# Performance work log

Hardware: AMD Instinct MI355X
Metric: run time of the kernel (lower is better)

## Reference

```python
import jax, jax.numpy as jnp
import numpy as np

EPS = 1e-6
BANDWIDTH = 10


def _norm_last(x):
    return x / jnp.sum(x, axis=-1, keepdims=True)


def _causal_linear_branch(Q, K, V, eps):
    # Q,K: [N,L,H,E] feature-mapped; V: [N,L,H,D]
    Q = _norm_last(Q)
    K = _norm_last(K)
    Kcum = jnp.cumsum(K, axis=1)                                   # [N,L,H,E]
    Z = 1.0 / (jnp.einsum('nlhe,nlhe->nlh', Q, Kcum) + eps)        # [N,L,H]
    # causal_dot_product: running sum of outer products K_s V_s^T
    S = jnp.cumsum(K[..., :, None] * V[..., None, :], axis=1)       # [N,L,H,E,D]
    Vn = jnp.einsum('nlhe,nlhed->nlhd', Q, S)                       # [N,L,H,D]
    return Vn * Z[..., None]


def setup_inputs() -> dict:
    key = jax.random.key(0)
    k1, k2, k3, k4 = jax.random.split(key, 4)
    N, L, H, E = 2, 2048, 8, 32
    return {
        'queries': jax.random.normal(k1, (N, L, H, E), dtype=jnp.float32),
        'keys': jax.random.normal(k2, (N, L, H, E), dtype=jnp.float32),
        'values': jax.random.normal(k3, (N, L, H, E), dtype=jnp.float32),
        'key_lengths': jnp.ones((N, L), dtype=jnp.float32),
        'W1': 0.02 * jax.random.normal(k4, (1, 1, H, E), dtype=jnp.float32),
        'W2': jnp.ones((1, 1, H, E), dtype=jnp.float32) * 0.5,
        'W3': jnp.ones((1, 1, H, E), dtype=jnp.float32) * 0.5,
    }


def reference(queries, keys, values, key_lengths, W1, W2, W3):
    klen = key_lengths[:, :, None, None]
    # kernel 1: elu feature map phi(x) = elu(x) + 1
    Q1 = jax.nn.elu(queries) + 1.0
    K1 = (jax.nn.elu(keys) + 1.0) * klen
    LV = W2 * _causal_linear_branch(Q1, K1, values, EPS)
    # kernel 2: squared elu feature map phi(x) = (elu(x) + 1)^2
    Q2 = (jax.nn.elu(queries) + 1.0) ** 2
    K2 = ((jax.nn.elu(keys) + 1.0) ** 2) * klen
    LV = LV + W3 * _causal_linear_branch(Q2, K2, values, EPS)
    # sparse near-field: banded causal softmax attention
    N, L, H, E = queries.shape
    temp = 1.0 / np.sqrt(E).astype(np.float32)
    QK = jnp.einsum('nlhe,nshe->nhls', queries * temp, keys)       # [N,H,L,S]
    li = jnp.arange(L)[:, None]
    si = jnp.arange(L)[None, :]
    band = (si <= li) & (si > li - BANDWIDTH)                      # keep band of width `bandwidth`
    QK = jnp.where(band[None, None], QK, -jnp.inf)
    A = jax.nn.softmax(QK, axis=-1)                                # dropout is identity (p=0 / eval)
    SV = jnp.einsum('nhls,nshd->nlhd', A, values)
    return W1 * SV + LV
```

## Files before the change

### kernel.cpp

```cpp
#include <hip/hip_runtime.h>
#include <cmath>

constexpr int NN = 2;
constexpr int LL = 2048;
constexpr int HH = 8;
constexpr int EE = 32;
constexpr int CC = 32;
constexpr int NCH = LL / CC;
constexpr int NB  = NN * HH * NCH;
constexpr int BWD = 10;
constexpr float EPSF = 1e-6f;
constexpr int REC  = 2 * (EE * EE + EE);
constexpr int REC4 = REC / 4;
constexpr int OFF_S1 = 0, OFF_K1 = 1024, OFF_S2 = 1056, OFF_K2 = 2080;
constexpr int SK = EE + 4;
constexpr int SB = 40;

using f32x16 = __attribute__((ext_vector_type(16))) float;
using s16x8  = __attribute__((ext_vector_type(8)))  short;

__device__ __forceinline__ float elu1(float x) {
    return x > 0.f ? x + 1.f : __expf(x);
}
__device__ __forceinline__ unsigned short bfr(float x) {
    union { float f; unsigned u; } v; v.f = x;
    return (unsigned short)((v.u + 0x7FFFu + ((v.u >> 16) & 1u)) >> 16);
}
__device__ __forceinline__ float bf2f(unsigned short b) {
    union { unsigned u; float f; } v; v.u = ((unsigned)b) << 16;
    return v.f;
}

__global__ __launch_bounds__(256) void chunksum_kernel(
    const float* __restrict__ Kin, const float* __restrict__ Vin,
    float* __restrict__ ws)
{
    __shared__ float K1n[CC][SK];
    __shared__ float K2n[CC][SK];
    __shared__ float Vs [CC][SK];

    const int b  = blockIdx.x;
    const int c  = b & (NCH - 1);
    const int nh = b >> 6;
    const int t  = threadIdx.x;
    const int lane = t & 31;
    const int grp  = t >> 5;

    for (int r = grp; r < CC; r += 8) {
        const int l = c * CC + r;
        const int base = ((nh >> 3) * LL + l) * HH * EE + (nh & 7) * EE + lane;
        const float k = Kin[base];
        const float v = Vin[base];
        const float f1 = elu1(k);
        const float f2 = f1 * f1;
        float s1 = f1, s2 = f2;
        #pragma unroll
        for (int m = 1; m < 32; m <<= 1) {
            s1 += __shfl_xor(s1, m, 32);
            s2 += __shfl_xor(s2, m, 32);
        }
        K1n[r][lane] = f1 / s1;
        K2n[r][lane] = f2 / s2;
        Vs [r][lane] = v;
    }
    __syncthreads();

    const int e  = t >> 3;
    const int d0 = (t & 7) * 4;
    float4 a1 = {0.f, 0.f, 0.f, 0.f};
    float4 a2 = {0.f, 0.f, 0.f, 0.f};
    float ks1 = 0.f, ks2 = 0.f;
    for (int j = 0; j < CC; ++j) {
        const float k1 = K1n[j][e];
        const float k2 = K2n[j][e];
        const float4 v = *(const float4*)&Vs[j][d0];
        ks1 += k1; ks2 += k2;
        a1.x += k1 * v.x; a1.y += k1 * v.y; a1.z += k1 * v.z; a1.w += k1 * v.w;
        a2.x += k2 * v.x; a2.y += k2 * v.y; a2.z += k2 * v.z; a2.w += k2 * v.w;
    }
    float* wb = ws + (size_t)b * REC;
    *(float4*)&wb[OFF_S1 + e * EE + d0] = a1;
    *(float4*)&wb[OFF_S2 + e * EE + d0] = a2;
    if ((t & 7) == 0) {
        wb[OFF_K1 + e] = ks1;
        wb[OFF_K2 + e] = ks2;
    }
}

__global__ __launch_bounds__(192) void prefix_kernel(float* __restrict__ ws)
{
    const int g = blockIdx.x / 11;
    const int e = (blockIdx.x % 11) * 192 + threadIdx.x;
    float* base = ws + (size_t)g * NCH * REC + e;
    float run = 0.f;
    {
        float v[32];
        #pragma unroll
        for (int c = 0; c < 32; ++c) v[c] = base[(size_t)c * REC];
        #pragma unroll
        for (int c = 0; c < 32; ++c) {
            const float x = v[c];
            base[(size_t)c * REC] = run;
            run += x;
        }
    }
    {
        float v[32];
        #pragma unroll
        for (int c = 0; c < 32; ++c) v[c] = base[(size_t)(32 + c) * REC];
        #pragma unroll
        for (int c = 0; c < 32; ++c) {
            const float x = v[c];
            base[(size_t)(32 + c) * REC] = run;
            run += x;
        }
    }
}

__global__ __launch_bounds__(256) void fused_kernel(
    const float* __restrict__ Qin, const float* __restrict__ Kin,
    const float* __restrict__ Vin,
    const float* __restrict__ W1, const float* __restrict__ W2,
    const float* __restrict__ W3, const float* __restrict__ ws,
    float* __restrict__ out)
{
    __shared__ float Vs [CC + 9][SK];
    __shared__ float qi1[CC], qi2[CC];
    __shared__ __align__(16) unsigned short Qfb [CC][SB];
    __shared__ __align__(16) unsigned short K1nb[CC][SB];
    __shared__ __align__(16) unsigned short K2nb[CC][SB];
    __shared__ __align__(16) unsigned short Pb1 [CC][SB];
    __shared__ __align__(16) unsigned short Pb2 [CC][SB];
    __shared__ float Ob1[CC][SK];
    __shared__ float Ob2[CC][SK];
    __shared__ __align__(16) union {
        float kr[(CC + 9) * SK];
        float sp[REC];
    } U;

    const int b  = blockIdx.x;
    const int c  = b & (NCH - 1);
    const int nh = b >> 6;
    const int h  = nh & 7;
    const int n  = nh >> 3;
    const int l0 = c * CC;
    const int t  = threadIdx.x;
    const int lane = t & 31;
    const int grp  = t >> 5;

    const float4* wbv = (const float4*)(ws + (size_t)b * REC);
    const float4 s0 = wbv[t];
    const float4 s1 = wbv[256 + t];
    float4 s2 = {0.f, 0.f, 0.f, 0.f};
    if (t < REC4 - 512) s2 = wbv[512 + t];

    for (int r = grp; r < CC; r += 8) {
        const int l = l0 + r;
        const int base = ((n * LL + l) * HH + h) * EE + lane;
        const float k = Kin[base];
        const float v = Vin[base];
        const float q = Qin[base];
        const float fk = elu1(k), fk2 = fk * fk;
        const float fq = elu1(q), fq2 = fq * fq;
        float sk1 = fk, sk2 = fk2, sq1 = fq, sq2 = fq2;
        #pragma unroll
        for (int m = 1; m < 32; m <<= 1) {
            sk1 += __shfl_xor(sk1, m, 32);
            sk2 += __shfl_xor(sk2, m, 32);
            sq1 += __shfl_xor(sq1, m, 32);
            sq2 += __shfl_xor(sq2, m, 32);
        }
        const float is1 = __builtin_amdgcn_rcpf(sk1);
        const float is2 = __builtin_amdgcn_rcpf(sk2);
        Qfb [r][lane] = bfr(fq);
        K1nb[r][lane] = bfr(fk  * is1);
        K2nb[r][lane] = bfr(fk2 * is2);
        Vs[9 + r][lane] = v;
        U.kr[(9 + r) * SK + lane] = k;
        if (lane == 0) {
            qi1[r] = 1.f / sq1; qi2[r] = 1.f / sq2;
        }
    }
    for (int idx = t; idx < 9 * 32; idx += 256) {
        const int rr = idx >> 5, ln = idx & 31;
        const int l = l0 - 9 + rr;
        float kv = 0.f, vv = 0.f;
        if (l >= 0) {
            const int gbase = ((n * LL + l) * HH + h) * EE + ln;
            kv = Kin[gbase];
            vv = Vin[gbase];
        }
        U.kr[rr * SK + ln] = kv;
        Vs[rr][ln] = vv;
    }

    const int r   = t >> 3;
    const int sub = t & 7;
    const int d0  = sub * 4;
    const int l   = l0 + r;

    const float4 q4 = *(const float4*)&Qin[((n * LL + l) * HH + h) * EE + d0];
    __syncthreads();

    float bnd[4];
    {
        const float temp = 0.17677669529663687f;
        float mx = -INFINITY, den = 0.f;
        float sv0 = 0.f, sv1 = 0.f, sv2 = 0.f, sv3 = 0.f;
        #pragma unroll
        for (int jj = 0; jj < BWD; ++jj) {
            const int j = l - (BWD - 1) + jj;
            if (j >= 0) {
                const float4 k4 = *(const float4*)&U.kr[(r + jj) * SK + d0];
                float p = q4.x*k4.x + q4.y*k4.y + q4.z*k4.z + q4.w*k4.w;
                p += __shfl_xor(p, 1, 8); p += __shfl_xor(p, 2, 8); p += __shfl_xor(p, 4, 8);
                const float s  = p * temp;
                const float mn = fmaxf(mx, s);
                const float c1 = __expf(mx - mn);
                const float c2 = __expf(s - mn);
                const float4 v4 = *(const float4*)&Vs[r + jj][d0];
                den = den * c1 + c2;
                sv0 = sv0 * c1 + c2 * v4.x;
                sv1 = sv1 * c1 + c2 * v4.y;
                sv2 = sv2 * c1 + c2 * v4.z;
                sv3 = sv3 * c1 + c2 * v4.w;
                mx = mn;
            }
        }
        const float inv = 1.f / den;
        const float4 w1 = *(const float4*)&W1[h * EE + d0];
        bnd[0] = w1.x * sv0 * inv; bnd[1] = w1.y * sv1 * inv;
        bnd[2] = w1.z * sv2 * inv; bnd[3] = w1.w * sv3 * inv;
    }
    __syncthreads();

    ((float4*)U.sp)[t]       = s0;
    ((float4*)U.sp)[256 + t] = s1;
    if (t < REC4 - 512) ((float4*)U.sp)[512 + t] = s2;
    __syncthreads();

    const int wid = t >> 6;
    const int l64 = t & 63;
    const int l31 = l64 & 31;
    const int hi5 = l64 >> 5;

    if ((wid & 1) == 0) {
        const bool b2 = (wid == 2);
        const unsigned short* Kn = b2 ? &K2nb[0][0] : &K1nb[0][0];
        const float* Sp  = U.sp + (b2 ? OFF_S2 : OFF_S1);
        const float* kp  = U.sp + (b2 ? OFF_K2 : OFF_K1);
        const float* qiv = b2 ? qi2 : qi1;
        const float* Wv  = b2 ? W3  : W2;
        unsigned short* Pb = b2 ? &Pb2[0][0] : &Pb1[0][0];
        float* Ob = b2 ? &Ob2[0][0] : &Ob1[0][0];

        s16x8 qa0 = *(const s16x8*)&Qfb[l31][8 * hi5];
        s16x8 qa1 = *(const s16x8*)&Qfb[l31][16 + 8 * hi5];
        if (b2) {
            #pragma unroll
            for (int i = 0; i < 8; ++i) {
                const float f0 = bf2f((unsigned short)qa0[i]);
                const float f1 = bf2f((unsigned short)qa1[i]);
                qa0[i] = (short)bfr(f0 * f0);
                qa1[i] = (short)bfr(f1 * f1);
            }
        }
        const s16x8 kb0 = *(const s16x8*)&Kn[l31 * SB + 8 * hi5];
        const s16x8 kb1 = *(const s16x8*)&Kn[l31 * SB + 16 + 8 * hi5];

        f32x16 P = {};
        P = __builtin_amdgcn_mfma_f32_32x32x16_bf16(qa0, kb0, P, 0, 0, 0);
        P = __builtin_amdgcn_mfma_f32_32x32x16_bf16(qa1, kb1, P, 0, 0, 0);

        #pragma unroll
        for (int k = 0; k < 16; ++k) {
            const int row = (k & 3) + 8 * (k >> 2) + 4 * hi5;
            const float pv = (l31 <= row) ? P[k] : 0.f;
            Pb[row * SB + l31] = bfr(pv);
        }
        const s16x8 pa0 = *(const s16x8*)&Pb[l31 * SB + 8 * hi5];
        const s16x8 pa1 = *(const s16x8*)&Pb[l31 * SB + 16 + 8 * hi5];

        s16x8 vb0, vb1;
        #pragma unroll
        for (int i = 0; i < 8; ++i) {
            vb0[i] = (short)bfr(Vs[9 + 8 * hi5 + i][l31]);
            vb1[i] = (short)bfr(Vs[9 + 16 + 8 * hi5 + i][l31]);
        }
        s16x8 sb0, sb1;
        #pragma unroll
        for (int i = 0; i < 8; ++i) {
            sb0[i] = (short)bfr(Sp[(8 * hi5 + i) * EE + l31]);
            sb1[i] = (short)bfr(Sp[(16 + 8 * hi5 + i) * EE + l31]);
        }
        f32x16 A = {};
        A = __builtin_amdgcn_mfma_f32_32x32x16_bf16(pa0, vb0, A, 0, 0, 0);
        A = __builtin_amdgcn_mfma_f32_32x32x16_bf16(pa1, vb1, A, 0, 0, 0);
        A = __builtin_amdgcn_mfma_f32_32x32x16_bf16(qa0, sb0, A, 0, 0, 0);
        A = __builtin_amdgcn_mfma_f32_32x32x16_bf16(qa1, sb1, A, 0, 0, 0);

        s16x8 ones;
        #pragma unroll
        for (int i = 0; i < 8; ++i) ones[i] = (short)0x3F80;
        s16x8 rb0, rb1;
        #pragma unroll
        for (int i = 0; i < 8; ++i) {
            rb0[i] = (short)bfr(kp[8 * hi5 + i]);
            rb1[i] = (short)bfr(kp[16 + 8 * hi5 + i]);
        }
        f32x16 Dp = {};
        Dp = __builtin_amdgcn_mfma_f32_32x32x16_bf16(pa0, ones, Dp, 0, 0, 0);
        Dp = __builtin_amdgcn_mfma_f32_32x32x16_bf16(pa1, ones, Dp, 0, 0, 0);
        Dp = __builtin_amdgcn_mfma_f32_32x32x16_bf16(qa0, rb0, Dp, 0, 0, 0);
        Dp = __builtin_amdgcn_mfma_f32_32x32x16_bf16(qa1, rb1, Dp, 0, 0, 0);

        const float wv = Wv[h * EE + l31];
        #pragma unroll
        for (int k = 0; k < 16; ++k) {
            const int row = (k & 3) + 8 * (k >> 2) + 4 * hi5;
            const float qi = qiv[row];
            const float z  = qi / (qi * Dp[k] + EPSF);
            Ob[row * SK + l31] = wv * A[k] * z;
        }
    }
    __syncthreads();

    const float4 o1 = *(const float4*)&Ob1[r][d0];
    const float4 o2 = *(const float4*)&Ob2[r][d0];
    float4 o;
    o.x = bnd[0] + o1.x + o2.x;
    o.y = bnd[1] + o1.y + o2.y;
    o.z = bnd[2] + o1.z + o2.z;
    o.w = bnd[3] + o1.w + o2.w;
    *(float4*)&out[((n * LL + l) * HH + h) * EE + d0] = o;
}

extern "C" void kernel_launch(void* const* d_in, const int* in_sizes, int n_in,
                              void* d_out, int out_size, void* d_ws, size_t ws_size,
                              hipStream_t stream)
{
    (void)in_sizes; (void)n_in; (void)out_size; (void)ws_size;
    const float* Q  = (const float*)d_in[0];
    const float* K  = (const float*)d_in[1];
    const float* V  = (const float*)d_in[2];
    const float* W1 = (const float*)d_in[4];
    const float* W2 = (const float*)d_in[5];
    const float* W3 = (const float*)d_in[6];
    float* out = (float*)d_out;
    float* ws  = (float*)d_ws;

    chunksum_kernel<<<NB,           256, 0, stream>>>(K, V, ws);
    prefix_kernel  <<<NN * HH * 11, 192, 0, stream>>>(ws);
    fused_kernel   <<<NB,           256, 0, stream>>>(Q, K, V, W1, W2, W3, ws, out);
}
```

Before: 102.0 us.

## Store chunk state in bf16 and fold query normalisation algebraically

The per-chunk KV state and key sums now go to the workspace as bf16, with the state transposed so the fused kernel can load MFMA operands directly instead of converting floats element by element. The query normalisation is removed because it cancels between numerator and denominator, and the eps term is dropped. Key normalisation inside the chunk is now done with an MFMA row-sum instead of warp shuffles. This halves workspace traffic and cuts shuffle and conversion work, at the cost of bf16 rounding in the prefix accumulation and a small change in numerics from dropping eps.

Result: no change. 101.6 us (-0.4%).

```diff
diff --git a/kernel.cpp b/kernel.cpp
--- a/kernel.cpp
+++ b/kernel.cpp
@@ -9,9 +9,8 @@
 constexpr int NCH = LL / CC;
 constexpr int NB  = NN * HH * NCH;
 constexpr int BWD = 10;
-constexpr float EPSF = 1e-6f;
 constexpr int REC  = 2 * (EE * EE + EE);
-constexpr int REC4 = REC / 4;
+constexpr int R16  = REC * 2 / 16;
 constexpr int OFF_S1 = 0, OFF_K1 = 1024, OFF_S2 = 1056, OFF_K2 = 2080;
 constexpr int SK = EE + 4;
 constexpr int SB = 40;
@@ -33,7 +32,7 @@
 
 __global__ __launch_bounds__(256) void chunksum_kernel(
     const float* __restrict__ Kin, const float* __restrict__ Vin,
-    float* __restrict__ ws)
+    unsigned short* __restrict__ ws)
 {
     __shared__ float K1n[CC][SK];
     __shared__ float K2n[CC][SK];
@@ -59,60 +58,64 @@
             s1 += __shfl_xor(s1, m, 32);
             s2 += __shfl_xor(s2, m, 32);
         }
-        K1n[r][lane] = f1 / s1;
-        K2n[r][lane] = f2 / s2;
+        K1n[r][lane] = f1 * __builtin_amdgcn_rcpf(s1);
+        K2n[r][lane] = f2 * __builtin_amdgcn_rcpf(s2);
         Vs [r][lane] = v;
     }
     __syncthreads();
 
-    const int e  = t >> 3;
-    const int d0 = (t & 7) * 4;
-    float4 a1 = {0.f, 0.f, 0.f, 0.f};
-    float4 a2 = {0.f, 0.f, 0.f, 0.f};
-    float ks1 = 0.f, ks2 = 0.f;
+    const int d  = t >> 3;
+    const int e0 = (t & 7) * 4;
+    float a1x=0.f,a1y=0.f,a1z=0.f,a1w=0.f;
+    float a2x=0.f,a2y=0.f,a2z=0.f,a2w=0.f;
+    float k1x=0.f,k1y=0.f,k1z=0.f,k1w=0.f;
+    float k2x=0.f,k2y=0.f,k2z=0.f,k2w=0.f;
     for (int j = 0; j < CC; ++j) {
-        const float k1 = K1n[j][e];
-        const float k2 = K2n[j][e];
-        const float4 v = *(const float4*)&Vs[j][d0];
-        ks1 += k1; ks2 += k2;
-        a1.x += k1 * v.x; a1.y += k1 * v.y; a1.z += k1 * v.z; a1.w += k1 * v.w;
-        a2.x += k2 * v.x; a2.y += k2 * v.y; a2.z += k2 * v.z; a2.w += k2 * v.w;
-    }
-    float* wb = ws + (size_t)b * REC;
-    *(float4*)&wb[OFF_S1 + e * EE + d0] = a1;
-    *(float4*)&wb[OFF_S2 + e * EE + d0] = a2;
-    if ((t & 7) == 0) {
-        wb[OFF_K1 + e] = ks1;
-        wb[OFF_K2 + e] = ks2;
-    }
-}
-
-__global__ __launch_bounds__(192) void prefix_kernel(float* __restrict__ ws)
+        const float vv = Vs[j][d];
+        const float4 k1 = *(const float4*)&K1n[j][e0];
+        const float4 k2 = *(const float4*)&K2n[j][e0];
+        k1x += k1.x; k1y += k1.y; k1z += k1.z; k1w += k1.w;
+        k2x += k2.x; k2y += k2.y; k2z += k2.z; k2w += k2.w;
+        a1x += vv * k1.x; a1y += vv * k1.y; a1z += vv * k1.z; a1w += vv * k1.w;
+        a2x += vv * k2.x; a2y += vv * k2.y; a2z += vv * k2.z; a2w += vv * k2.w;
+    }
+    unsigned short* wb = ws + (size_t)b * REC;
+    ushort4 o1 = { bfr(a1x), bfr(a1y), bfr(a1z), bfr(a1w) };
+    ushort4 o2 = { bfr(a2x), bfr(a2y), bfr(a2z), bfr(a2w) };
+    *(ushort4*)&wb[OFF_S1 + d * EE + e0] = o1;
+    *(ushort4*)&wb[OFF_S2 + d * EE + e0] = o2;
+    if (d == 0) {
+        ushort4 s1v = { bfr(k1x), bfr(k1y), bfr(k1z), bfr(k1w) };
+        ushort4 s2v = { bfr(k2x), bfr(k2y), bfr(k2z), bfr(k2w) };
+        *(ushort4*)&wb[OFF_K1 + e0] = s1v;
+        *(ushort4*)&wb[OFF_K2 + e0] = s2v;
+    }
+}
+
+__global__ __launch_bounds__(192) void prefix_kernel(unsigned short* __restrict__ ws)
 {
     const int g = blockIdx.x / 11;
     const int e = (blockIdx.x % 11) * 192 + threadIdx.x;
-    float* base = ws + (size_t)g * NCH * REC + e;
+    unsigned short* base = ws + (size_t)g * NCH * REC + e;
     float run = 0.f;
     {
-        float v[32];
+        unsigned short v[32];
         #pragma unroll
         for (int c = 0; c < 32; ++c) v[c] = base[(size_t)c * REC];
         #pragma unroll
         for (int c = 0; c < 32; ++c) {
-            const float x = v[c];
-            base[(size_t)c * REC] = run;
-            run += x;
+            base[(size_t)c * REC] = bfr(run);
+            run += bf2f(v[c]);
         }
     }
     {
-        float v[32];
+        unsigned short v[32];
         #pragma unroll
         for (int c = 0; c < 32; ++c) v[c] = base[(size_t)(32 + c) * REC];
         #pragma unroll
         for (int c = 0; c < 32; ++c) {
-            const float x = v[c];
-            base[(size_t)(32 + c) * REC] = run;
-            run += x;
+            base[(size_t)(32 + c) * REC] = bfr(run);
+            run += bf2f(v[c]);
         }
     }
 }
@@ -121,21 +124,19 @@
     const float* __restrict__ Qin, const float* __restrict__ Kin,
     const float* __restrict__ Vin,
     const float* __restrict__ W1, const float* __restrict__ W2,
-    const float* __restrict__ W3, const float* __restrict__ ws,
+    const float* __restrict__ W3, const unsigned short* __restrict__ ws,
     float* __restrict__ out)
 {
     __shared__ float Vs [CC + 9][SK];
-    __shared__ float qi1[CC], qi2[CC];
-    __shared__ __align__(16) unsigned short Qfb [CC][SB];
-    __shared__ __align__(16) unsigned short K1nb[CC][SB];
-    __shared__ __align__(16) unsigned short K2nb[CC][SB];
-    __shared__ __align__(16) unsigned short Pb1 [CC][SB];
-    __shared__ __align__(16) unsigned short Pb2 [CC][SB];
+    __shared__ __align__(16) unsigned short Qfb[CC][SB];
+    __shared__ __align__(16) unsigned short Kfb[CC][SB];
+    __shared__ __align__(16) unsigned short Pb1[CC][SB];
+    __shared__ __align__(16) unsigned short Pb2[CC][SB];
     __shared__ float Ob1[CC][SK];
     __shared__ float Ob2[CC][SK];
     __shared__ __align__(16) union {
         float kr[(CC + 9) * SK];
-        float sp[REC];
+        unsigned short sp[REC];
     } U;
 
     const int b  = blockIdx.x;
@@ -148,11 +149,10 @@
     const int lane = t & 31;
     const int grp  = t >> 5;
 
-    const float4* wbv = (const float4*)(ws + (size_t)b * REC);
-    const float4 s0 = wbv[t];
-    const float4 s1 = wbv[256 + t];
-    float4 s2 = {0.f, 0.f, 0.f, 0.f};
-    if (t < REC4 - 512) s2 = wbv[512 + t];
+    const uint4* wbv = (const uint4*)(ws + (size_t)b * REC);
+    const uint4 s0 = wbv[t];
+    uint4 s1 = {0u, 0u, 0u, 0u};
+    if (t < R16 - 256) s1 = wbv[256 + t];
 
     for (int r = grp; r < CC; r += 8) {
         const int l = l0 + r;
@@ -160,26 +160,10 @@
         const float k = Kin[base];
         const float v = Vin[base];
         const float q = Qin[base];
-        const float fk = elu1(k), fk2 = fk * fk;
-        const float fq = elu1(q), fq2 = fq * fq;
-        float sk1 = fk, sk2 = fk2, sq1 = fq, sq2 = fq2;
-        #pragma unroll
-        for (int m = 1; m < 32; m <<= 1) {
-            sk1 += __shfl_xor(sk1, m, 32);
-            sk2 += __shfl_xor(sk2, m, 32);
-            sq1 += __shfl_xor(sq1, m, 32);
-            sq2 += __shfl_xor(sq2, m, 32);
-        }
-        const float is1 = __builtin_amdgcn_rcpf(sk1);
-        const float is2 = __builtin_amdgcn_rcpf(sk2);
-        Qfb [r][lane] = bfr(fq);
-        K1nb[r][lane] = bfr(fk  * is1);
-        K2nb[r][lane] = bfr(fk2 * is2);
+        Kfb[r][lane] = bfr(elu1(k));
+        Qfb[r][lane] = bfr(elu1(q));
         Vs[9 + r][lane] = v;
         U.kr[(9 + r) * SK + lane] = k;
-        if (lane == 0) {
-            qi1[r] = 1.f / sq1; qi2[r] = 1.f / sq2;
-        }
     }
     for (int idx = t; idx < 9 * 32; idx += 256) {
         const int rr = idx >> 5, ln = idx & 31;
@@ -234,9 +218,8 @@
     }
     __syncthreads();
 
-    ((float4*)U.sp)[t]       = s0;
-    ((float4*)U.sp)[256 + t] = s1;
-    if (t < REC4 - 512) ((float4*)U.sp)[512 + t] = s2;
+    ((uint4*)U.sp)[t] = s0;
+    if (t < R16 - 256) ((uint4*)U.sp)[256 + t] = s1;
     __syncthreads();
 
     const int wid = t >> 6;
@@ -246,37 +229,42 @@
 
     if ((wid & 1) == 0) {
         const bool b2 = (wid == 2);
-        const unsigned short* Kn = b2 ? &K2nb[0][0] : &K1nb[0][0];
-        const float* Sp  = U.sp + (b2 ? OFF_S2 : OFF_S1);
-        const float* kp  = U.sp + (b2 ? OFF_K2 : OFF_K1);
-        const float* qiv = b2 ? qi2 : qi1;
-        const float* Wv  = b2 ? W3  : W2;
+        const unsigned short* Spt = U.sp + (b2 ? OFF_S2 : OFF_S1);
+        const unsigned short* kp  = U.sp + (b2 ? OFF_K2 : OFF_K1);
+        const float* Wv = b2 ? W3 : W2;
         unsigned short* Pb = b2 ? &Pb2[0][0] : &Pb1[0][0];
         float* Ob = b2 ? &Ob2[0][0] : &Ob1[0][0];
 
         s16x8 qa0 = *(const s16x8*)&Qfb[l31][8 * hi5];
         s16x8 qa1 = *(const s16x8*)&Qfb[l31][16 + 8 * hi5];
+        s16x8 kb0 = *(const s16x8*)&Kfb[l31][8 * hi5];
+        s16x8 kb1 = *(const s16x8*)&Kfb[l31][16 + 8 * hi5];
         if (b2) {
             #pragma unroll
             for (int i = 0; i < 8; ++i) {
-                const float f0 = bf2f((unsigned short)qa0[i]);
-                const float f1 = bf2f((unsigned short)qa1[i]);
-                qa0[i] = (short)bfr(f0 * f0);
-                qa1[i] = (short)bfr(f1 * f1);
+                float f;
+                f = bf2f((unsigned short)qa0[i]); qa0[i] = (short)bfr(f * f);
+                f = bf2f((unsigned short)qa1[i]); qa1[i] = (short)bfr(f * f);
+                f = bf2f((unsigned short)kb0[i]); kb0[i] = (short)bfr(f * f);
+                f = bf2f((unsigned short)kb1[i]); kb1[i] = (short)bfr(f * f);
             }
         }
-        const s16x8 kb0 = *(const s16x8*)&Kn[l31 * SB + 8 * hi5];
-        const s16x8 kb1 = *(const s16x8*)&Kn[l31 * SB + 16 + 8 * hi5];
-
+        s16x8 ones;
+        #pragma unroll
+        for (int i = 0; i < 8; ++i) ones[i] = (short)0x3F80;
+
+        f32x16 Dk = {};
+        Dk = __builtin_amdgcn_mfma_f32_32x32x16_bf16(ones, kb0, Dk, 0, 0, 0);
+        Dk = __builtin_amdgcn_mfma_f32_32x32x16_bf16(ones, kb1, Dk, 0, 0, 0);
         f32x16 P = {};
         P = __builtin_amdgcn_mfma_f32_32x32x16_bf16(qa0, kb0, P, 0, 0, 0);
         P = __builtin_amdgcn_mfma_f32_32x32x16_bf16(qa1, kb1, P, 0, 0, 0);
 
+        const float ki = __builtin_amdgcn_rcpf(Dk[0]);
         #pragma unroll
         for (int k = 0; k < 16; ++k) {
             const int row = (k & 3) + 8 * (k >> 2) + 4 * hi5;
-            const float pv = (l31 <= row) ? P[k] : 0.f;
-            Pb[row * SB + l31] = bfr(pv);
+            Pb[row * SB + l31] = bfr((l31 <= row) ? P[k] * ki : 0.f);
         }
         const s16x8 pa0 = *(const s16x8*)&Pb[l31 * SB + 8 * hi5];
         const s16x8 pa1 = *(const s16x8*)&Pb[l31 * SB + 16 + 8 * hi5];
@@ -287,27 +275,17 @@
             vb0[i] = (short)bfr(Vs[9 + 8 * hi5 + i][l31]);
             vb1[i] = (short)bfr(Vs[9 + 16 + 8 * hi5 + i][l31]);
         }
-        s16x8 sb0, sb1;
-        #pragma unroll
-        for (int i = 0; i < 8; ++i) {
-            sb0[i] = (short)bfr(Sp[(8 * hi5 + i) * EE + l31]);
-            sb1[i] = (short)bfr(Sp[(16 + 8 * hi5 + i) * EE + l31]);
-        }
+        const s16x8 sb0 = *(const s16x8*)&Spt[l31 * EE + 8 * hi5];
+        const s16x8 sb1 = *(const s16x8*)&Spt[l31 * EE + 16 + 8 * hi5];
+        const s16x8 rb0 = *(const s16x8*)&kp[8 * hi5];
+        const s16x8 rb1 = *(const s16x8*)&kp[16 + 8 * hi5];
+
         f32x16 A = {};
         A = __builtin_amdgcn_mfma_f32_32x32x16_bf16(pa0, vb0, A, 0, 0, 0);
         A = __builtin_amdgcn_mfma_f32_32x32x16_bf16(pa1, vb1, A, 0, 0, 0);
         A = __builtin_amdgcn_mfma_f32_32x32x16_bf16(qa0, sb0, A, 0, 0, 0);
         A = __builtin_amdgcn_mfma_f32_32x32x16_bf16(qa1, sb1, A, 0, 0, 0);
 
-        s16x8 ones;
-        #pragma unroll
-        for (int i = 0; i < 8; ++i) ones[i] = (short)0x3F80;
-        s16x8 rb0, rb1;
-        #pragma unroll
-        for (int i = 0; i < 8; ++i) {
-            rb0[i] = (short)bfr(kp[8 * hi5 + i]);
-            rb1[i] = (short)bfr(kp[16 + 8 * hi5 + i]);
-        }
         f32x16 Dp = {};
         Dp = __builtin_amdgcn_mfma_f32_32x32x16_bf16(pa0, ones, Dp, 0, 0, 0);
         Dp = __builtin_amdgcn_mfma_f32_32x32x16_bf16(pa1, ones, Dp, 0, 0, 0);
@@ -318,9 +296,7 @@
         #pragma unroll
         for (int k = 0; k < 16; ++k) {
             const int row = (k & 3) + 8 * (k >> 2) + 4 * hi5;
-            const float qi = qiv[row];
-            const float z  = qi / (qi * Dp[k] + EPSF);
-            Ob[row * SK + l31] = wv * A[k] * z;
+            Ob[row * SK + l31] = wv * A[k] * __builtin_amdgcn_rcpf(Dp[k]);
         }
     }
     __syncthreads();
@@ -347,7 +323,7 @@
     const float* W2 = (const float*)d_in[5];
     const float* W3 = (const float*)d_in[6];
     float* out = (float*)d_out;
-    float* ws  = (float*)d_ws;
+    unsigned short* ws = (unsigned short*)d_ws;
 
     chunksum_kernel<<<NB,           256, 0, stream>>>(K, V, ws);
     prefix_kernel  <<<NN * HH * 11, 192, 0, stream>>>(ws);
```
